# Performance work log

Hardware: AMD Instinct MI355X
Metric: run time of the kernel (lower is better)

The kernel has to match this reference:

```python
import jax, jax.numpy as jnp
import numpy as np

B, N, K, H = 8192, 512, 8, 1024  # batch, size_half, n_segments, hidden width


def setup_inputs() -> dict:
    key = jax.random.key(0)
    ks = jax.random.split(key, 8)
    out_dim = N * (2 * K + 1)  # 8704
    v_in = jax.random.uniform(ks[0], (B, 2 * N), jnp.float32)  # in [0,1]
    log_density = jax.random.uniform(ks[1], (B, 1), jnp.float32)
    W1 = jax.random.normal(ks[2], (N, H), jnp.float32) / np.float32(np.sqrt(N))
    b1 = jnp.zeros((H,), jnp.float32)
    W2 = jax.random.normal(ks[3], (H, H), jnp.float32) / np.float32(np.sqrt(H))
    b2 = jnp.zeros((H,), jnp.float32)
    W3 = jax.random.normal(ks[4], (H, out_dim), jnp.float32) / np.float32(np.sqrt(H))
    b3 = jnp.zeros((out_dim,), jnp.float32)
    return {"v_in": v_in, "log_density": log_density,
            "W1": W1, "b1": b1, "W2": W2, "b2": b2, "W3": W3, "b3": b3}


def reference(v_in, log_density, W1, b1, W2, b2, W3, b3):
    v_passive = v_in[:, :N]   # even_sites=True -> passive first
    v_active = v_in[:, N:]
    # fully connected net, tanh on every layer (no_final_activation=False)
    x = jnp.tanh((v_passive - 0.5) @ W1 + b1)
    x = jnp.tanh(x @ W2 + b2)
    x = jnp.tanh(x @ W3 + b3)
    net = x.reshape(B, N, 2 * K + 1)
    h_net, w_net = net[..., : K + 1], net[..., K + 1 :]
    w_norm = jax.nn.softmax(w_net, axis=2)                          # (B,N,K)
    eh = jnp.exp(h_net)                                             # (B,N,K+1)
    denom = (0.5 * w_norm * (eh[..., :-1] + eh[..., 1:])).sum(axis=2, keepdims=True)
    h_norm = eh / denom                                             # (B,N,K+1)
    zeros = jnp.zeros((B, N, 1), v_in.dtype)
    knots_x = jnp.concatenate([zeros, jnp.cumsum(w_norm, axis=2)], axis=2)  # (B,N,K+1)
    knots_y = jnp.concatenate(
        [zeros, jnp.cumsum(0.5 * w_norm * (h_norm[..., :-1] + h_norm[..., 1:]), axis=2)],
        axis=2)                                                     # (B,N,K+1)
    # left-searchsorted(knots_x, v_active) == count of knots strictly below v
    k = jnp.clip(jnp.sum(knots_x < v_active[..., None], axis=2) - 1, 0, K - 1)  # (B,N)
    idx = k[..., None]
    w_seg = jnp.take_along_axis(w_norm, idx, axis=2)[..., 0]
    h_lo = jnp.take_along_axis(h_norm, idx, axis=2)[..., 0]
    h_hi = jnp.take_along_axis(h_norm, idx + 1, axis=2)[..., 0]
    x_lo = jnp.take_along_axis(knots_x, idx, axis=2)[..., 0]
    y_lo = jnp.take_along_axis(knots_y, idx, axis=2)[..., 0]
    alpha = (v_active - x_lo) / w_seg
    v_active_out = y_lo + alpha * h_lo * w_seg + 0.5 * alpha ** 2 * (h_hi - h_lo) * w_seg
    v_out = jnp.concatenate([v_passive, v_active_out], axis=1)      # (B,2N)
    log_density_out = log_density - jnp.log(h_lo + alpha * (h_hi - h_lo)).sum(axis=1, keepdims=True)
    return v_out, log_density_out
```

## Files before the change

kernel.cpp:

```cpp
#include <hip/hip_runtime.h>
#include <math.h>

#define BB    8192
#define NN    512
#define KKN   8
#define HH    1024
#define OUTD  (NN * (2 * KKN + 1))

typedef unsigned short ushort_t;
typedef __bf16 bf16x8 __attribute__((ext_vector_type(8)));
typedef float  f32x16 __attribute__((ext_vector_type(16)));
typedef float  f32x4  __attribute__((ext_vector_type(4)));
typedef int    i32x4  __attribute__((ext_vector_type(4)));
typedef float  f32x2v __attribute__((ext_vector_type(2)));

__device__ inline ushort_t f2bf(float f) {
    unsigned int u = __float_as_uint(f);
    unsigned int r = (u + 0x7fffu + ((u >> 16) & 1u)) >> 16;
    return (ushort_t)r;
}
__device__ inline float bf2f(ushort_t u) {
    return __uint_as_float(((unsigned int)u) << 16);
}

__device__ inline float fast_tanh(float x) {
    float t = __expf(x + x);
    return fmaf(-2.f, __builtin_amdgcn_rcpf(t + 1.f), 1.f);
}

__global__ __launch_bounds__(256) void conv_v(
    const float* __restrict__ v_in, ushort_t* __restrict__ a0b)
{
    int t = blockIdx.x * 256 + threadIdx.x;
    int e0 = t * 2;
    int b = e0 >> 9;
    int n = e0 & 511;
    const float2 v = *(const float2*)(v_in + (size_t)b * (2 * NN) + n);
    ushort_t* o = a0b + (size_t)b * NN + n;
    o[0] = f2bf(v.x - 0.5f);
    o[1] = f2bf(v.y - 0.5f);
}

template <bool PERM>
__global__ __launch_bounds__(256) void transpose_cvt(
    const float* __restrict__ W, ushort_t* __restrict__ WT, int Kd, int Nd)
{
    __shared__ float tile[32][33];
    const int bx = blockIdx.x * 32;
    const int by = blockIdx.y * 32;
    const int tx = threadIdx.x;
    const int ty = threadIdx.y;
#pragma unroll
    for (int i = 0; i < 32; i += 8)
        tile[ty + i][tx] = W[(size_t)(by + ty + i) * Nd + bx + tx];
    __syncthreads();
#pragma unroll
    for (int i = 0; i < 32; i += 8) {
        int r = bx + ty + i;
        if (PERM) r = (r % 17) * 512 + (r / 17);
        WT[(size_t)r * Kd + by + tx] = f2bf(tile[tx][ty + i]);
    }
}

template <bool PERM_BIAS>
__global__ __launch_bounds__(256) void gemm_bt_tanh(
    const ushort_t* __restrict__ A,
    const ushort_t* __restrict__ BT,
    const float* __restrict__ bias,
    ushort_t* __restrict__ C,
    int N_, int K)
{
    __shared__ __align__(16) ushort_t sA[128 * 32];
    __shared__ __align__(16) ushort_t sB[128 * 32];

    const int t    = threadIdx.x;
    const int lane = t & 63;
    const int w    = t >> 6;
    const int wy   = w >> 1;
    const int wx   = w & 1;
    const int l31  = lane & 31;
    const int h    = lane >> 5;

    const int brow = blockIdx.y * 128;
    const int bcol = blockIdx.x * 128;

    f32x16 acc[2][2] = {};

    const int cwb = (t & ~63);

    int rS[2], gS[2];
#pragma unroll
    for (int p = 0; p < 2; ++p) {
        const int c = p * 256 + t;
        rS[p] = c >> 2;
        gS[p] = ((c & 3) - (rS[p] >> 1)) & 3;
    }

    int offA[2][2], offB[2][2];
#pragma unroll
    for (int ks = 0; ks < 2; ++ks)
#pragma unroll
        for (int ti = 0; ti < 2; ++ti) {
            const int rA = wy * 64 + ti * 32 + l31;
            offA[ks][ti] = rA * 32 + ((2 * ks + h + (rA >> 1)) & 3) * 8;
            const int rB = wx * 64 + ti * 32 + l31;
            offB[ks][ti] = rB * 32 + ((2 * ks + h + (rB >> 1)) & 3) * 8;
        }

    for (int k0 = 0; k0 < K; k0 += 32) {
        __syncthreads();
#pragma unroll
        for (int p = 0; p < 2; ++p) {
            const int cb = p * 256 + cwb;
            const ushort_t* ga = A  + (size_t)(brow + rS[p]) * K + k0 + gS[p] * 8;
            const ushort_t* gb = BT + (size_t)(bcol + rS[p]) * K + k0 + gS[p] * 8;
            __builtin_amdgcn_global_load_lds(
                (const __attribute__((address_space(1))) void*)ga,
                (__attribute__((address_space(3))) void*)(sA + (size_t)cb * 8), 16, 0, 0);
            __builtin_amdgcn_global_load_lds(
                (const __attribute__((address_space(1))) void*)gb,
                (__attribute__((address_space(3))) void*)(sB + (size_t)cb * 8), 16, 0, 0);
        }
        __syncthreads();

#pragma unroll
        for (int ks = 0; ks < 2; ++ks) {
            const bf16x8 a0 = *(const bf16x8*)(sA + offA[ks][0]);
            const bf16x8 a1 = *(const bf16x8*)(sA + offA[ks][1]);
            const bf16x8 b0 = *(const bf16x8*)(sB + offB[ks][0]);
            const bf16x8 b1 = *(const bf16x8*)(sB + offB[ks][1]);
            acc[0][0] = __builtin_amdgcn_mfma_f32_32x32x16_bf16(a0, b0, acc[0][0], 0, 0, 0);
            acc[0][1] = __builtin_amdgcn_mfma_f32_32x32x16_bf16(a0, b1, acc[0][1], 0, 0, 0);
            acc[1][0] = __builtin_amdgcn_mfma_f32_32x32x16_bf16(a1, b0, acc[1][0], 0, 0, 0);
            acc[1][1] = __builtin_amdgcn_mfma_f32_32x32x16_bf16(a1, b1, acc[1][1], 0, 0, 0);
        }
    }

#pragma unroll
    for (int tj = 0; tj < 2; ++tj) {
        const int col = bcol + wx * 64 + tj * 32 + l31;
        const int bidx = PERM_BIAS ? ((col & 511) * 17 + (col >> 9)) : col;
        const float bv = bias[bidx];
#pragma unroll
        for (int ti = 0; ti < 2; ++ti) {
            const int rb = brow + wy * 64 + ti * 32 + 4 * h;
#pragma unroll
            for (int reg = 0; reg < 16; ++reg) {
                const int row = rb + (reg & 3) + 8 * (reg >> 2);
                C[(size_t)row * N_ + col] = f2bf(fast_tanh(acc[ti][tj][reg] + bv));
            }
        }
    }
}

__device__ __forceinline__ void stage16(
    const ushort_t* __restrict__ gsrc, ushort_t* lds_dst)
{
    __builtin_amdgcn_global_load_lds(
        (const __attribute__((address_space(1))) void*)gsrc,
        (__attribute__((address_space(3))) void*)lds_dst, 16, 0, 0);
}

template <bool PERM_BIAS>
__global__ __launch_bounds__(512, 4) void gemm3_bt_tanh_128x256(
    const ushort_t* __restrict__ A,
    const ushort_t* __restrict__ BT,
    const float* __restrict__ bias,
    ushort_t* __restrict__ C,
    int N_, int K)
{
    __shared__ __align__(16) ushort_t smem[128 * 256];
    ushort_t* sA = smem;
    ushort_t* sB = smem + 4096;

    const int t    = threadIdx.x;
    const int lane = t & 63;
    const int w    = t >> 6;
    const int wy   = w >> 2;
    const int wx   = w & 3;
    const int l15  = lane & 15;
    const int kg   = lane >> 4;

    const int gx = gridDim.x, gy = gridDim.y;
    int br, bc;
    {
        const int o = blockIdx.y * gx + blockIdx.x;
        if ((gy & 7) == 0) {
            const int rpx = gy >> 3;
            const int xcd = o & 7;
            const int seq = o >> 3;
            const int bpg = rpx << 3;
            const int g   = seq / bpg;
            const int rem = seq % bpg;
            const int gcw = gx - g * 8;
            const int gw  = gcw < 8 ? gcw : 8;
            bc = g * 8 + rem % gw;
            br = xcd * rpx + rem / gw;
        } else {
            const int nwg = gx * gy;
            const int id = (o & 7) * (nwg >> 3) + (o >> 3);
            br = id / gx; bc = id % gx;
        }
    }
    const int brow = br * 128;
    const int bcol = bc * 256;

    f32x4 acc[4][4] = {};

    const int rT  = t >> 2;
    const int g8  = (((t & 3) ^ ((t >> 3) & 3)) << 3);
    const int wbU = (t & ~63) * 8;
    const size_t rowA  = (size_t)(brow + rT) * K;
    const size_t rowB0 = (size_t)(bcol + rT) * K;
    const size_t rowB1 = (size_t)(bcol + 128 + rT) * K;

    int offA[4], offB[4];
#pragma unroll
    for (int m = 0; m < 4; ++m) {
        const int r = wy * 64 + m * 16 + l15;
        offA[m] = r * 32 + (((kg ^ (r >> 1)) & 3) << 3);
    }
#pragma unroll
    for (int n = 0; n < 4; ++n) {
        const int r = wx * 64 + n * 16 + l15;
        offB[n] = r * 32 + (((kg ^ (r >> 1)) & 3) << 3);
    }

    for (int k0 = 0; k0 < K; k0 += 32) {
        __syncthreads();
        stage16(A  + rowA  + k0 + g8, sA + wbU);
        stage16(BT + rowB0 + k0 + g8, sB + wbU);
        stage16(BT + rowB1 + k0 + g8, sB + 4096 + wbU);
        __syncthreads();

        bf16x8 aR[4], bR[4];
#pragma unroll
        for (int n = 0; n < 4; ++n) bR[n] = *(const bf16x8*)(sB + offB[n]);
#pragma unroll
        for (int m = 0; m < 4; ++m) aR[m] = *(const bf16x8*)(sA + offA[m]);
#pragma unroll
        for (int m = 0; m < 4; ++m)
#pragma unroll
            for (int n = 0; n < 4; ++n)
                acc[m][n] = __builtin_amdgcn_mfma_f32_16x16x32_bf16(
                    aR[m], bR[n], acc[m][n], 0, 0, 0);
    }
    __syncthreads();

    ushort_t* sC = smem;
#pragma unroll
    for (int n = 0; n < 4; ++n) {
        const int cg  = wx * 64 + n * 16 + l15;
        const int col = bcol + cg;
        const int bidx = PERM_BIAS ? ((col & 511) * 17 + (col >> 9)) : col;
        const float bv = bias[bidx];
#pragma unroll
        for (int m = 0; m < 4; ++m) {
            const int rg0 = wy * 64 + m * 16 + kg * 4;
            const int cgs = cg ^ (((rg0 >> 2) & 3) << 4);
#pragma unroll
            for (int reg = 0; reg < 4; ++reg)
                sC[(rg0 + reg) * 256 + cgs] =
                    f2bf(fast_tanh(acc[m][n][reg] + bv));
        }
    }
    __syncthreads();

#pragma unroll
    for (int i = 0; i < 8; ++i) {
        const int slot = i * 512 + t;
        const int r  = slot >> 5;
        const int j  = slot & 31;
        const int js = j ^ (((r >> 2) & 3) << 1);
        *(i32x4*)(C + (size_t)(brow + r) * N_ + bcol + j * 8) =
            *(const i32x4*)(sC + r * 256 + js * 8);
    }
}

__global__ __launch_bounds__(256) void spline_post(
    const ushort_t* __restrict__ net,
    const float* __restrict__ v_in,
    const float* __restrict__ ld_in,
    float* __restrict__ v_out,
    float* __restrict__ ld_out)
{
    const int b = blockIdx.x;
    const int t = threadIdx.x;

    unsigned int pl[17];
    const ushort_t* base = net + (size_t)b * OUTD + 2 * t;
#pragma unroll
    for (int p = 0; p < 17; ++p)
        pl[p] = __builtin_nontemporal_load((const unsigned int*)(base + p * 512));

    {
        const f32x2v vp = __builtin_nontemporal_load(
            (const f32x2v*)(v_in + (size_t)b * (2 * NN) + 2 * t));
        __builtin_nontemporal_store(
            vp, (f32x2v*)(v_out + (size_t)b * (2 * NN) + 2 * t));
    }
    const f32x2v va2 = __builtin_nontemporal_load(
        (const f32x2v*)(v_in + (size_t)b * (2 * NN) + NN + 2 * t));

    float vact[2];
    float lt_sum = 0.f;
#pragma unroll 1
    for (int u = 0; u < 2; ++u) {
        const int sh = u * 16;
        float t17[17];
#pragma unroll
        for (int p = 0; p < 17; ++p)
            t17[p] = bf2f((ushort_t)(pl[p] >> sh));

        float m = t17[9];
#pragma unroll
        for (int i = 10; i < 17; i++) m = fmaxf(m, t17[i]);
        float wn[8], wsum = 0.f;
#pragma unroll
        for (int i = 0; i < 8; i++) { wn[i] = __expf(t17[9 + i] - m); wsum += wn[i]; }
        const float winv = 1.f / wsum;
#pragma unroll
        for (int i = 0; i < 8; i++) wn[i] *= winv;

        float eh[9];
#pragma unroll
        for (int i = 0; i < 9; i++) eh[i] = __expf(t17[i]);
        float denom = 0.f;
#pragma unroll
        for (int k = 0; k < 8; k++) denom += 0.5f * wn[k] * (eh[k] + eh[k + 1]);
        const float dinv = 1.f / denom;
        float hn[9];
#pragma unroll
        for (int i = 0; i < 9; i++) hn[i] = eh[i] * dinv;

        float kx[9], ky[9];
        kx[0] = 0.f; ky[0] = 0.f;
#pragma unroll
        for (int k = 0; k < 8; k++) {
            kx[k + 1] = kx[k] + wn[k];
            ky[k + 1] = ky[k] + 0.5f * wn[k] * (hn[k] + hn[k + 1]);
        }

        const float va = (u == 0) ? va2.x : va2.y;
        int cnt = 0;
#pragma unroll
        for (int j = 0; j < 9; j++) cnt += (kx[j] < va) ? 1 : 0;
        int k = cnt - 1;
        k = k < 0 ? 0 : (k > KKN - 1 ? KKN - 1 : k);

        const float wseg = wn[k];
        const float hlo = hn[k], hhi = hn[k + 1];
        const float xlo = kx[k], ylo = ky[k];
        const float alpha = (va - xlo) / wseg;
        vact[u] = ylo + alpha * hlo * wseg + 0.5f * alpha * alpha * (hhi - hlo) * wseg;
        lt_sum += __logf(hlo + alpha * (hhi - hlo));
    }

    {
        f32x2v vo; vo.x = vact[0]; vo.y = vact[1];
        __builtin_nontemporal_store(
            vo, (f32x2v*)(v_out + (size_t)b * (2 * NN) + NN + 2 * t));
    }

    __shared__ float wred[4];
#pragma unroll
    for (int o = 32; o > 0; o >>= 1) lt_sum += __shfl_down(lt_sum, o, 64);
    if ((t & 63) == 0) wred[t >> 6] = lt_sum;
    __syncthreads();
    if (t == 0)
        ld_out[b] = ld_in[b] - (wred[0] + wred[1] + wred[2] + wred[3]);
}

extern "C" void kernel_launch(void* const* d_in, const int* in_sizes, int n_in,
                              void* d_out, int out_size, void* d_ws, size_t ws_size,
                              hipStream_t stream)
{
    const float* v_in = (const float*)d_in[0];
    const float* ld   = (const float*)d_in[1];
    const float* W1   = (const float*)d_in[2];
    const float* b1   = (const float*)d_in[3];
    const float* W2   = (const float*)d_in[4];
    const float* b2   = (const float*)d_in[5];
    const float* W3   = (const float*)d_in[6];
    const float* b3   = (const float*)d_in[7];

    float* out    = (float*)d_out;
    float* v_out  = out;
    float* ld_out = out + (size_t)BB * (2 * NN);

    const size_t Mi = 1048576;
    int    chunk;
    size_t region;
    if      (ws_size >= 172 * Mi) { chunk = 8192; region = 136 * Mi; }
    else if (ws_size >= 104 * Mi) { chunk = 4096; region =  68 * Mi; }
    else if (ws_size >=  70 * Mi) { chunk = 2048; region =  34 * Mi; }
    else                          { chunk = 1024; region =  24 * Mi; }

    char* ws = (char*)d_ws;
    ushort_t* a0b = (ushort_t*)(ws);
    ushort_t* x1b = (ushort_t*)(ws + 8 * Mi);
    ushort_t* netc = (ushort_t*)(ws);
    ushort_t* x2b = (ushort_t*)(ws + region);
    ushort_t* W1T = (ushort_t*)(ws + region + 16 * Mi);
    ushort_t* W2T = (ushort_t*)(ws + region + 17 * Mi);
    ushort_t* W3T = (ushort_t*)(ws + region + 19 * Mi);

    conv_v<<<dim3(BB * NN / 2 / 256), dim3(256), 0, stream>>>(v_in, a0b);
    transpose_cvt<false><<<dim3(HH / 32, NN / 32),   dim3(32, 8), 0, stream>>>(W1, W1T, NN, HH);
    transpose_cvt<false><<<dim3(HH / 32, HH / 32),   dim3(32, 8), 0, stream>>>(W2, W2T, HH, HH);
    transpose_cvt<true ><<<dim3(OUTD / 32, HH / 32), dim3(32, 8), 0, stream>>>(W3, W3T, HH, OUTD);

    gemm_bt_tanh<false><<<dim3(HH / 128, BB / 128), dim3(256), 0, stream>>>(
        a0b, W1T, b1, x1b, HH, NN);
    gemm_bt_tanh<false><<<dim3(HH / 128, BB / 128), dim3(256), 0, stream>>>(
        x1b, W2T, b2, x2b, HH, HH);

    for (int c = 0; c < BB / chunk; ++c) {
        const ushort_t* xa = x2b + (size_t)c * chunk * HH;
        gemm3_bt_tanh_128x256<true><<<dim3(OUTD / 256, chunk / 128), dim3(512), 0, stream>>>(
            xa, W3T, b3, netc, OUTD, HH);
        spline_post<<<dim3(chunk), dim3(256), 0, stream>>>(
            netc,
            v_in   + (size_t)c * chunk * (2 * NN),
            ld     + (size_t)c * chunk,
            v_out  + (size_t)c * chunk * (2 * NN),
            ld_out + (size_t)c * chunk);
    }
}
```

Before: 395.3 us.

## Fuse third GEMM with spline epilogue, drop intermediate net buffer

Fuses the final GEMM with the rational-quadratic spline post-processing. Each block now computes a 128x272 tile covering 16 whole sites with 17 parameters each, using an extra MFMA column strip, and runs the spline directly from LDS. This removes the write and re-read of the large bf16 network output and the chunked launch loop. A separate kernel copies the passive half and initialises log density. The per-row log-density sum becomes atomic adds across blocks, which makes the summation order nondeterministic. The padded LDS tile, the partial 16-column strip done by every wave, and the spline work run per block may lower MFMA efficiency.

```diff
diff --git a/kernel.cpp b/kernel.cpp
--- a/kernel.cpp
+++ b/kernel.cpp
@@ -39,6 +39,18 @@
     ushort_t* o = a0b + (size_t)b * NN + n;
     o[0] = f2bf(v.x - 0.5f);
     o[1] = f2bf(v.y - 0.5f);
+}
+
+__global__ __launch_bounds__(256) void passive_ld_init(
+    const float* __restrict__ v_in, const float* __restrict__ ld_in,
+    float* __restrict__ v_out, float* __restrict__ ld_out)
+{
+    const int idx = blockIdx.x * 256 + threadIdx.x;
+    const int b = idx >> 8;
+    const int j = idx & 255;
+    const float2 vp = *(const float2*)(v_in + (size_t)b * (2 * NN) + 2 * j);
+    *(float2*)(v_out + (size_t)b * (2 * NN) + 2 * j) = vp;
+    if (j == 0) ld_out[b] = ld_in[b];
 }
 
 template <bool PERM>
@@ -161,15 +173,18 @@
         (__attribute__((address_space(3))) void*)lds_dst, 16, 0, 0);
 }
 
-template <bool PERM_BIAS>
-__global__ __launch_bounds__(512, 4) void gemm3_bt_tanh_128x256(
+#define CSTR 276
+
+__global__ __launch_bounds__(512, 4) void gemm3_spline_fused(
     const ushort_t* __restrict__ A,
     const ushort_t* __restrict__ BT,
     const float* __restrict__ bias,
-    ushort_t* __restrict__ C,
-    int N_, int K)
-{
-    __shared__ __align__(16) ushort_t smem[128 * 256];
+    const float* __restrict__ v_in,
+    float* __restrict__ v_out,
+    float* __restrict__ ld_out,
+    int K)
+{
+    __shared__ __align__(16) ushort_t smem[128 * CSTR];
     ushort_t* sA = smem;
     ushort_t* sB = smem + 4096;
 
@@ -202,19 +217,21 @@
             br = id / gx; bc = id % gx;
         }
     }
-    const int brow = br * 128;
-    const int bcol = bc * 256;
+    const int brow  = br * 128;
+    const int bcol0 = bc * 272;
 
     f32x4 acc[4][4] = {};
+    f32x4 acc2 = {};
 
     const int rT  = t >> 2;
     const int g8  = (((t & 3) ^ ((t >> 3) & 3)) << 3);
     const int wbU = (t & ~63) * 8;
-    const size_t rowA  = (size_t)(brow + rT) * K;
-    const size_t rowB0 = (size_t)(bcol + rT) * K;
-    const size_t rowB1 = (size_t)(bcol + 128 + rT) * K;
-
-    int offA[4], offB[4];
+    const size_t rowA  = (size_t)(brow  + rT) * K;
+    const size_t rowB0 = (size_t)(bcol0 + rT) * K;
+    const size_t rowB1 = (size_t)(bcol0 + 128 + rT) * K;
+    const size_t rowB2 = (size_t)(bcol0 + 256 + rT) * K;
+
+    int offA[4], offB[4], offB2;
 #pragma unroll
     for (int m = 0; m < 4; ++m) {
         const int r = wy * 64 + m * 16 + l15;
@@ -224,6 +241,10 @@
     for (int n = 0; n < 4; ++n) {
         const int r = wx * 64 + n * 16 + l15;
         offB[n] = r * 32 + (((kg ^ (r >> 1)) & 3) << 3);
+    }
+    {
+        const int r = 256 + l15;
+        offB2 = r * 32 + (((kg ^ (r >> 1)) & 3) << 3);
     }
 
     for (int k0 = 0; k0 < K; k0 += 32) {
@@ -231,6 +252,7 @@
         stage16(A  + rowA  + k0 + g8, sA + wbU);
         stage16(BT + rowB0 + k0 + g8, sB + wbU);
         stage16(BT + rowB1 + k0 + g8, sB + 4096 + wbU);
+        if (t < 64) stage16(BT + rowB2 + k0 + g8, sB + 8192);
         __syncthreads();
 
         bf16x8 aR[4], bR[4];
@@ -238,113 +260,86 @@
         for (int n = 0; n < 4; ++n) bR[n] = *(const bf16x8*)(sB + offB[n]);
 #pragma unroll
         for (int m = 0; m < 4; ++m) aR[m] = *(const bf16x8*)(sA + offA[m]);
+        const bf16x8 b2 = *(const bf16x8*)(sB + offB2);
 #pragma unroll
         for (int m = 0; m < 4; ++m)
 #pragma unroll
             for (int n = 0; n < 4; ++n)
                 acc[m][n] = __builtin_amdgcn_mfma_f32_16x16x32_bf16(
                     aR[m], bR[n], acc[m][n], 0, 0, 0);
+        acc2 = __builtin_amdgcn_mfma_f32_16x16x32_bf16(aR[wx], b2, acc2, 0, 0, 0);
     }
     __syncthreads();
 
-    ushort_t* sC = smem;
 #pragma unroll
     for (int n = 0; n < 4; ++n) {
-        const int cg  = wx * 64 + n * 16 + l15;
-        const int col = bcol + cg;
-        const int bidx = PERM_BIAS ? ((col & 511) * 17 + (col >> 9)) : col;
-        const float bv = bias[bidx];
+        const int col = wx * 64 + n * 16 + l15;
+        const float bv = bias[bcol0 + col];
 #pragma unroll
         for (int m = 0; m < 4; ++m) {
             const int rg0 = wy * 64 + m * 16 + kg * 4;
-            const int cgs = cg ^ (((rg0 >> 2) & 3) << 4);
 #pragma unroll
             for (int reg = 0; reg < 4; ++reg)
-                sC[(rg0 + reg) * 256 + cgs] =
+                smem[(rg0 + reg) * CSTR + col] =
                     f2bf(fast_tanh(acc[m][n][reg] + bv));
         }
     }
+    {
+        const int col = 256 + l15;
+        const float bv = bias[bcol0 + col];
+        const int rg0 = wy * 64 + wx * 16 + kg * 4;
+#pragma unroll
+        for (int reg = 0; reg < 4; ++reg)
+            smem[(rg0 + reg) * CSTR + col] =
+                f2bf(fast_tanh(acc2[reg] + bv));
+    }
     __syncthreads();
 
-#pragma unroll
-    for (int i = 0; i < 8; ++i) {
-        const int slot = i * 512 + t;
-        const int r  = slot >> 5;
-        const int j  = slot & 31;
-        const int js = j ^ (((r >> 2) & 3) << 1);
-        *(i32x4*)(C + (size_t)(brow + r) * N_ + bcol + j * 8) =
-            *(const i32x4*)(sC + r * 256 + js * 8);
-    }
-}
-
-__global__ __launch_bounds__(256) void spline_post(
-    const ushort_t* __restrict__ net,
-    const float* __restrict__ v_in,
-    const float* __restrict__ ld_in,
-    float* __restrict__ v_out,
-    float* __restrict__ ld_out)
-{
-    const int b = blockIdx.x;
-    const int t = threadIdx.x;
-
-    unsigned int pl[17];
-    const ushort_t* base = net + (size_t)b * OUTD + 2 * t;
-#pragma unroll
-    for (int p = 0; p < 17; ++p)
-        pl[p] = __builtin_nontemporal_load((const unsigned int*)(base + p * 512));
-
-    {
-        const f32x2v vp = __builtin_nontemporal_load(
-            (const f32x2v*)(v_in + (size_t)b * (2 * NN) + 2 * t));
-        __builtin_nontemporal_store(
-            vp, (f32x2v*)(v_out + (size_t)b * (2 * NN) + 2 * t));
-    }
-    const f32x2v va2 = __builtin_nontemporal_load(
-        (const f32x2v*)(v_in + (size_t)b * (2 * NN) + NN + 2 * t));
-
-    float vact[2];
-    float lt_sum = 0.f;
 #pragma unroll 1
-    for (int u = 0; u < 2; ++u) {
-        const int sh = u * 16;
+    for (int i = 0; i < 4; ++i) {
+        const int pair = i * 512 + t;
+        const int row  = pair >> 4;
+        const int u    = pair & 15;
+        const ushort_t* cp = smem + row * CSTR + u * 17;
+
         float t17[17];
 #pragma unroll
-        for (int p = 0; p < 17; ++p)
-            t17[p] = bf2f((ushort_t)(pl[p] >> sh));
-
-        float m = t17[9];
-#pragma unroll
-        for (int i = 10; i < 17; i++) m = fmaxf(m, t17[i]);
+        for (int j = 0; j < 17; ++j) t17[j] = bf2f(cp[j]);
+
+        float mx = t17[9];
+#pragma unroll
+        for (int j = 10; j < 17; ++j) mx = fmaxf(mx, t17[j]);
         float wn[8], wsum = 0.f;
 #pragma unroll
-        for (int i = 0; i < 8; i++) { wn[i] = __expf(t17[9 + i] - m); wsum += wn[i]; }
+        for (int j = 0; j < 8; ++j) { wn[j] = __expf(t17[9 + j] - mx); wsum += wn[j]; }
         const float winv = 1.f / wsum;
 #pragma unroll
-        for (int i = 0; i < 8; i++) wn[i] *= winv;
+        for (int j = 0; j < 8; ++j) wn[j] *= winv;
 
         float eh[9];
 #pragma unroll
-        for (int i = 0; i < 9; i++) eh[i] = __expf(t17[i]);
+        for (int j = 0; j < 9; ++j) eh[j] = __expf(t17[j]);
         float denom = 0.f;
 #pragma unroll
-        for (int k = 0; k < 8; k++) denom += 0.5f * wn[k] * (eh[k] + eh[k + 1]);
+        for (int k = 0; k < 8; ++k) denom += 0.5f * wn[k] * (eh[k] + eh[k + 1]);
         const float dinv = 1.f / denom;
         float hn[9];
 #pragma unroll
-        for (int i = 0; i < 9; i++) hn[i] = eh[i] * dinv;
+        for (int j = 0; j < 9; ++j) hn[j] = eh[j] * dinv;
 
         float kx[9], ky[9];
         kx[0] = 0.f; ky[0] = 0.f;
 #pragma unroll
-        for (int k = 0; k < 8; k++) {
+        for (int k = 0; k < 8; ++k) {
             kx[k + 1] = kx[k] + wn[k];
             ky[k + 1] = ky[k] + 0.5f * wn[k] * (hn[k] + hn[k + 1]);
         }
 
-        const float va = (u == 0) ? va2.x : va2.y;
+        const size_t vi = (size_t)(brow + row) * (2 * NN) + NN + bc * 16 + u;
+        const float va = v_in[vi];
         int cnt = 0;
 #pragma unroll
-        for (int j = 0; j < 9; j++) cnt += (kx[j] < va) ? 1 : 0;
+        for (int j = 0; j < 9; ++j) cnt += (kx[j] < va) ? 1 : 0;
         int k = cnt - 1;
         k = k < 0 ? 0 : (k > KKN - 1 ? KKN - 1 : k);
 
@@ -352,23 +347,15 @@
         const float hlo = hn[k], hhi = hn[k + 1];
         const float xlo = kx[k], ylo = ky[k];
         const float alpha = (va - xlo) / wseg;
-        vact[u] = ylo + alpha * hlo * wseg + 0.5f * alpha * alpha * (hhi - hlo) * wseg;
-        lt_sum += __logf(hlo + alpha * (hhi - hlo));
-    }
-
-    {
-        f32x2v vo; vo.x = vact[0]; vo.y = vact[1];
-        __builtin_nontemporal_store(
-            vo, (f32x2v*)(v_out + (size_t)b * (2 * NN) + NN + 2 * t));
-    }
-
-    __shared__ float wred[4];
-#pragma unroll
-    for (int o = 32; o > 0; o >>= 1) lt_sum += __shfl_down(lt_sum, o, 64);
-    if ((t & 63) == 0) wred[t >> 6] = lt_sum;
-    __syncthreads();
-    if (t == 0)
-        ld_out[b] = ld_in[b] - (wred[0] + wred[1] + wred[2] + wred[3]);
+        v_out[vi] = ylo + alpha * hlo * wseg
+                  + 0.5f * alpha * alpha * (hhi - hlo) * wseg;
+        float lt = __logf(hlo + alpha * (hhi - hlo));
+
+#pragma unroll
+        for (int o = 8; o > 0; o >>= 1) lt += __shfl_xor(lt, o, 16);
+        if ((t & 15) == 0)
+            atomicAdd(ld_out + brow + row, -lt);
+    }
 }
 
 extern "C" void kernel_launch(void* const* d_in, const int* in_sizes, int n_in,
@@ -389,41 +376,25 @@
     float* ld_out = out + (size_t)BB * (2 * NN);
 
     const size_t Mi = 1048576;
-    int    chunk;
-    size_t region;
-    if      (ws_size >= 172 * Mi) { chunk = 8192; region = 136 * Mi; }
-    else if (ws_size >= 104 * Mi) { chunk = 4096; region =  68 * Mi; }
-    else if (ws_size >=  70 * Mi) { chunk = 2048; region =  34 * Mi; }
-    else                          { chunk = 1024; region =  24 * Mi; }
-
     char* ws = (char*)d_ws;
     ushort_t* a0b = (ushort_t*)(ws);
     ushort_t* x1b = (ushort_t*)(ws + 8 * Mi);
-    ushort_t* netc = (ushort_t*)(ws);
-    ushort_t* x2b = (ushort_t*)(ws + region);
-    ushort_t* W1T = (ushort_t*)(ws + region + 16 * Mi);
-    ushort_t* W2T = (ushort_t*)(ws + region + 17 * Mi);
-    ushort_t* W3T = (ushort_t*)(ws + region + 19 * Mi);
+    ushort_t* x2b = (ushort_t*)(ws + 24 * Mi);
+    ushort_t* W1T = (ushort_t*)(ws + 40 * Mi);
+    ushort_t* W2T = (ushort_t*)(ws + 41 * Mi);
+    ushort_t* W3T = (ushort_t*)(ws + 43 * Mi);
 
     conv_v<<<dim3(BB * NN / 2 / 256), dim3(256), 0, stream>>>(v_in, a0b);
     transpose_cvt<false><<<dim3(HH / 32, NN / 32),   dim3(32, 8), 0, stream>>>(W1, W1T, NN, HH);
     transpose_cvt<false><<<dim3(HH / 32, HH / 32),   dim3(32, 8), 0, stream>>>(W2, W2T, HH, HH);
-    transpose_cvt<true ><<<dim3(OUTD / 32, HH / 32), dim3(32, 8), 0, stream>>>(W3, W3T, HH, OUTD);
+    transpose_cvt<false><<<dim3(OUTD / 32, HH / 32), dim3(32, 8), 0, stream>>>(W3, W3T, HH, OUTD);
 
     gemm_bt_tanh<false><<<dim3(HH / 128, BB / 128), dim3(256), 0, stream>>>(
         a0b, W1T, b1, x1b, HH, NN);
     gemm_bt_tanh<false><<<dim3(HH / 128, BB / 128), dim3(256), 0, stream>>>(
         x1b, W2T, b2, x2b, HH, HH);
 
-    for (int c = 0; c < BB / chunk; ++c) {
-        const ushort_t* xa = x2b + (size_t)c * chunk * HH;
-        gemm3_bt_tanh_128x256<true><<<dim3(OUTD / 256, chunk / 128), dim3(512), 0, stream>>>(
-            xa, W3T, b3, netc, OUTD, HH);
-        spline_post<<<dim3(chunk), dim3(256), 0, stream>>>(
-            netc,
-            v_in   + (size_t)c * chunk * (2 * NN),
-            ld     + (size_t)c * chunk,
-            v_out  + (size_t)c * chunk * (2 * NN),
-            ld_out + (size_t)c * chunk);
-    }
-}
+    passive_ld_init<<<dim3(BB), dim3(256), 0, stream>>>(v_in, ld, v_out, ld_out);
+    gemm3_spline_fused<<<dim3(NN / 16, BB / 128), dim3(512), 0, stream>>>(
+        x2b, W3T, b3, v_in, v_out, ld_out, HH);
+}
```

Measured after the change: 593.9 us. 50.2% more time.
